# Kernel optimization log

Hardware: AMD Instinct MI355X
Metric: run time of the kernel (lower is better)

Reference implementation:

```python
import jax, jax.numpy as jnp
import numpy as np

INPUT_DIM = 1024
OUTPUT_DIM = 1024
NUM_SEGMENTS = 8
GRID_LO, GRID_HI = -1.0, 1.0


def setup_inputs() -> dict:
    key = jax.random.key(0)
    k1, k2 = jax.random.split(key)
    x = jax.random.normal(k1, (8, 2048, INPUT_DIM), dtype=jnp.float32)
    coeff = jax.random.normal(k2, (NUM_SEGMENTS + 1, OUTPUT_DIM, INPUT_DIM), dtype=jnp.float32) * 0.1
    bias = jnp.zeros((OUTPUT_DIM,), dtype=jnp.float32)
    return {"x": x, "coeff": coeff, "bias": bias}


def reference(x, coeff, bias):
    # x: (..., I); coeff: (G, O, I) with G = num_segments + 1; bias: (O,)
    batch_shape = x.shape[:-1]
    x_flat = x.reshape(-1, INPUT_DIM)                      # (B, I)
    grid = jnp.linspace(GRID_LO, GRID_HI, NUM_SEGMENTS + 1, dtype=x.dtype)  # (G,)
    h = (GRID_HI - GRID_LO) / NUM_SEGMENTS

    x_mean = jnp.mean(x_flat, axis=-1, keepdims=True)      # (B, 1)
    diff = x_mean - grid[None, :]                          # (B, G)
    w = jax.nn.relu(1.0 - jnp.abs(diff) / h)               # triangular hat weights
    w = w / (jnp.sum(w, axis=-1, keepdims=True) + 1e-8)    # (B, G)

    # Fused contraction order: avoid the (B, O, I) intermediate of the
    # original einsum chain; same math by associativity.
    t = jnp.einsum('bi,goi->bgo', x_flat, coeff)           # (B, G, O)
    out = jnp.einsum('bg,bgo->bo', w, t) + bias            # (B, O)
    return out.reshape(*batch_shape, OUTPUT_DIM)
```

## Files before the change

kernel.cpp:

```cpp
#include <hip/hip_runtime.h>
#include <math.h>

#define B_ROWS 16384
#define IDIM   1024
#define ODIM   1024
#define NGRID  9
#define MT_MAX 137
#define MPAD_MAX (MT_MAX*128)

#define RS_BLOCKS 256
#define RS_ROWS   (B_ROWS / RS_BLOCKS)

typedef __attribute__((ext_vector_type(8))) short frag8;
typedef __attribute__((ext_vector_type(4))) float f32x4;

typedef __attribute__((address_space(1))) void gvoid;
typedef __attribute__((address_space(3))) void lvoid;

__device__ __forceinline__ void async_cp16(const void* g, void* l) {
  __builtin_amdgcn_global_load_lds((gvoid*)(void*)g, (lvoid*)l, 16, 0, 0);
}

__device__ __forceinline__ unsigned short f2bf(float f) {
  union { float f; unsigned u; } v; v.f = f;
  unsigned u = v.u;
  u += 0x7fffu + ((u >> 16) & 1u);
  return (unsigned short)(u >> 16);
}

__device__ __forceinline__ void seg_weights(float m, int& sI, float& w0, float& w1) {
  float wsum = 0.f, wg[NGRID];
#pragma unroll
  for (int g = 0; g < NGRID; g++) {
    float gv = -1.f + 0.25f * (float)g;
    float t = 1.f - fabsf(m - gv) * 4.f;
    wg[g] = t > 0.f ? t : 0.f;
    wsum += wg[g];
  }
  int s = (int)floorf((m + 1.f) * 4.f);
  s = s < 0 ? 0 : (s > 7 ? 7 : s);
  float inv = 1.f / (wsum + 1e-8f);
  sI = s;
  w0 = wg[s] * inv;
  w1 = wg[s + 1] * inv;
}

__global__ void zero_meta(int* bucket_cnt) {
  if (threadIdx.x < NGRID) bucket_cnt[threadIdx.x] = 0;
}

__global__ void row_stats(const float* __restrict__ x, float* __restrict__ w0a,
                          float* __restrict__ w1a, int* __restrict__ sidx,
                          int* __restrict__ rank, int* __restrict__ bucket_cnt) {
  __shared__ int lcnt[NGRID];
  __shared__ int base[NGRID];
  __shared__ int lrank[RS_ROWS];
  __shared__ int lseg[RS_ROWS];
  const int tid  = threadIdx.x;
  const int lane = tid & 63;
  const int wave = tid >> 6;
  if (tid < NGRID) lcnt[tid] = 0;
  __syncthreads();
  const int row0 = blockIdx.x * RS_ROWS;
#pragma unroll 4
  for (int it = 0; it < RS_ROWS / 4; ++it) {
    int r = it * 4 + wave;
    int b = row0 + r;
    const float4* xr = (const float4*)(x + (size_t)b * IDIM);
    float s = 0.f;
#pragma unroll
    for (int j = 0; j < 4; j++) {
      float4 v = xr[lane + j * 64];
      s += v.x + v.y + v.z + v.w;
    }
#pragma unroll
    for (int off = 32; off; off >>= 1) s += __shfl_down(s, off, 64);
    if (lane == 0) {
      float m = s * (1.0f / (float)IDIM);
      int sI; float w0, w1;
      seg_weights(m, sI, w0, w1);
      w0a[b] = w0; w1a[b] = w1; sidx[b] = sI;
      lseg[r] = sI;
      lrank[r] = atomicAdd(&lcnt[sI], 1);
    }
  }
  __syncthreads();
  if (tid < NGRID) base[tid] = lcnt[tid] ? atomicAdd(&bucket_cnt[tid], lcnt[tid]) : 0;
  __syncthreads();
  if (tid < RS_ROWS) rank[row0 + tid] = base[lseg[tid]] + lrank[tid];
}

__global__ void plan_kernel(const int* __restrict__ cnt, int* __restrict__ bucket_off,
                            int* __restrict__ tile_seg, int* __restrict__ row_idx) {
  __shared__ int offs[NGRID + 1];
  const int tid = threadIdx.x;
  if (tid == 0) {
    int off = 0;
    for (int g = 0; g < NGRID; g++) {
      offs[g] = off;
      off += ((cnt[g] + 127) >> 7) << 7;
    }
    offs[NGRID] = off;
  }
  __syncthreads();
  if (tid < NGRID) bucket_off[tid] = offs[tid];
  for (int t = tid; t < MT_MAX; t += 256) {
    int seg = -1;
#pragma unroll
    for (int g = 0; g < NGRID; g++)
      if (t >= (offs[g] >> 7) && t < (offs[g + 1] >> 7)) seg = g;
    tile_seg[t] = seg;
  }
#pragma unroll
  for (int g = 0; g < NGRID; g++) {
    int lo = offs[g] + cnt[g], hi = offs[g + 1];
    for (int p = lo + tid; p < hi; p += 256) row_idx[p] = -1;
  }
}

#define BA_ROWS 8
__global__ void build_a(const float* __restrict__ x, const float* __restrict__ w0a,
                        const float* __restrict__ w1a, const int* __restrict__ sidx,
                        const int* __restrict__ rank, const int* __restrict__ bucket_off,
                        unsigned short* __restrict__ Xs, float2* __restrict__ ws,
                        int* __restrict__ row_idx) {
  const int tid = threadIdx.x;
  const int b0 = blockIdx.x * BA_ROWS;
#pragma unroll
  for (int r = 0; r < BA_ROWS; r++) {
    int b = b0 + r;
    int s = sidx[b];
    int p = bucket_off[s] + rank[b];
    if (tid == 0) { row_idx[p] = b; ws[p] = make_float2(w0a[b], w1a[b]); }
    float4 v = ((const float4*)(x + (size_t)b * IDIM))[tid];
    ushort4 u;
    u.x = f2bf(v.x); u.y = f2bf(v.y); u.z = f2bf(v.z); u.w = f2bf(v.w);
    *(ushort4*)(Xs + (size_t)p * IDIM + tid * 4) = u;
  }
}

__global__ void cvt_coeff(const float* __restrict__ c, unsigned short* __restrict__ cb, int n4) {
  int i = blockIdx.x * blockDim.x + threadIdx.x;
  if (i < n4) {
    float4 v = ((const float4*)c)[i];
    ushort4 o;
    o.x = f2bf(v.x); o.y = f2bf(v.y); o.z = f2bf(v.z); o.w = f2bf(v.w);
    ((ushort4*)cb)[i] = o;
  }
}

__global__ void __launch_bounds__(256, 2)
kan_gemm(const unsigned short* __restrict__ Xs,
         const unsigned short* __restrict__ Cb,
         const int* __restrict__ row_idx,
         const int* __restrict__ tile_seg,
         const float2* __restrict__ ws,
         const float* __restrict__ bias,
         float* __restrict__ out) {
  int seg = tile_seg[blockIdx.y];
  if (seg < 0) return;
  __shared__ unsigned short As[128 * 32];
  __shared__ unsigned short Bs0[128 * 32];
  __shared__ unsigned short Bs1[128 * 32];

  const int tid  = threadIdx.x;
  const int lane = tid & 63;
  const int wave = tid >> 6;
  const int wm   = wave >> 1;
  const int wn   = wave & 1;
  const size_t rowA0 = (size_t)blockIdx.y * 128;
  const int    colB0 = blockIdx.x * 128;

  const int lrow = lane >> 2;
  const int lk8  = (lane & 3) * 8;

  const unsigned short* gA  = Xs + (rowA0 + lrow) * IDIM + lk8;
  const unsigned short* gB0 = Cb + ((size_t)(seg * ODIM + colB0 + lrow)) * IDIM + lk8;
  const unsigned short* gB1 = gB0 + (size_t)ODIM * IDIM;

  f32x4 acc0[4][4] = {};
  f32x4 acc1[4][4] = {};

  for (int kk = 0; kk < IDIM; kk += 32) {
    __syncthreads();
#pragma unroll
    for (int t = 0; t < 2; t++) {
      int r0 = (wave * 2 + t) * 16;
      async_cp16(gA  + (size_t)r0 * IDIM + kk, &As[r0 * 32]);
      async_cp16(gB0 + (size_t)r0 * IDIM + kk, &Bs0[r0 * 32]);
      async_cp16(gB1 + (size_t)r0 * IDIM + kk, &Bs1[r0 * 32]);
    }
    __syncthreads();

    frag8 af[4], bfr[4];
#pragma unroll
    for (int mi = 0; mi < 4; mi++)
      af[mi] = *(const frag8*)&As[(wm * 64 + mi * 16 + (lane & 15)) * 32 + (lane >> 4) * 8];
#pragma unroll
    for (int ni = 0; ni < 4; ni++)
      bfr[ni] = *(const frag8*)&Bs0[(wn * 64 + ni * 16 + (lane & 15)) * 32 + (lane >> 4) * 8];
#pragma unroll
    for (int mi = 0; mi < 4; mi++)
#pragma unroll
      for (int ni = 0; ni < 4; ni++)
        acc0[mi][ni] = __builtin_amdgcn_mfma_f32_16x16x32_bf16(af[mi], bfr[ni], acc0[mi][ni], 0, 0, 0);
#pragma unroll
    for (int ni = 0; ni < 4; ni++)
      bfr[ni] = *(const frag8*)&Bs1[(wn * 64 + ni * 16 + (lane & 15)) * 32 + (lane >> 4) * 8];
#pragma unroll
    for (int mi = 0; mi < 4; mi++)
#pragma unroll
      for (int ni = 0; ni < 4; ni++)
        acc1[mi][ni] = __builtin_amdgcn_mfma_f32_16x16x32_bf16(af[mi], bfr[ni], acc1[mi][ni], 0, 0, 0);
  }

  int   col[4]; float bv[4];
#pragma unroll
  for (int ni = 0; ni < 4; ni++) {
    col[ni] = colB0 + wn * 64 + ni * 16 + (lane & 15);
    bv[ni]  = bias[col[ni]];
  }
#pragma unroll
  for (int mi = 0; mi < 4; mi++) {
    int prow = (int)rowA0 + wm * 64 + mi * 16 + (lane >> 4) * 4;
#pragma unroll
    for (int r = 0; r < 4; r++) {
      int p = prow + r;
      int orow = row_idx[p];
      if ((unsigned)orow < (unsigned)B_ROWS) {
        float2 w = ws[p];
        float* o = out + (size_t)orow * ODIM;
#pragma unroll
        for (int ni = 0; ni < 4; ni++)
          o[col[ni]] = w.x * acc0[mi][ni][r] + w.y * acc1[mi][ni][r] + bv[ni];
      }
    }
  }
}

__global__ void fallback_kernel(const float* __restrict__ x, const float* __restrict__ coeff,
                                const float* __restrict__ bias, float* __restrict__ out) {
  int b = blockIdx.x;
  int tid = threadIdx.x;
  __shared__ float xs[IDIM];
  __shared__ float ps[4];
  __shared__ float mw[2];
  __shared__ int   ms;
  float4 v = ((const float4*)(x + (size_t)b * IDIM))[tid];
  ((float4*)xs)[tid] = v;
  float s = v.x + v.y + v.z + v.w;
#pragma unroll
  for (int off = 32; off; off >>= 1) s += __shfl_down(s, off, 64);
  if ((tid & 63) == 0) ps[tid >> 6] = s;
  __syncthreads();
  if (tid == 0) {
    float m = (ps[0] + ps[1] + ps[2] + ps[3]) * (1.0f / (float)IDIM);
    int sI; float w0, w1;
    seg_weights(m, sI, w0, w1);
    mw[0] = w0; mw[1] = w1; ms = sI;
  }
  __syncthreads();
  float w0 = mw[0], w1 = mw[1]; int sI = ms;
  for (int o = tid; o < ODIM; o += 256) {
    const float* c0 = coeff + ((size_t)sI * ODIM + o) * IDIM;
    const float* c1 = c0 + (size_t)ODIM * IDIM;
    float a0 = 0.f, a1 = 0.f;
    for (int i = 0; i < IDIM; i++) { a0 += xs[i] * c0[i]; a1 += xs[i] * c1[i]; }
    out[(size_t)b * ODIM + o] = w0 * a0 + w1 * a1 + bias[o];
  }
}

extern "C" void kernel_launch(void* const* d_in, const int* in_sizes, int n_in,
                              void* d_out, int out_size, void* d_ws, size_t ws_size,
                              hipStream_t stream) {
  const float* x     = (const float*)d_in[0];
  const float* coeff = (const float*)d_in[1];
  const float* bias  = (const float*)d_in[2];
  float* out = (float*)d_out;

  size_t szXs = (size_t)MPAD_MAX * IDIM * sizeof(unsigned short);
  size_t szCb = (size_t)NGRID * ODIM * IDIM * sizeof(unsigned short);
  size_t o0 = 0;
  unsigned short* Xs = (unsigned short*)((char*)d_ws + o0); o0 += szXs;
  unsigned short* Cb = (unsigned short*)((char*)d_ws + o0); o0 += szCb;
  float2* ws = (float2*)((char*)d_ws + o0); o0 += (size_t)MPAD_MAX * 8;
  float* w0a = (float*)((char*)d_ws + o0); o0 += (size_t)B_ROWS * 4;
  float* w1a = (float*)((char*)d_ws + o0); o0 += (size_t)B_ROWS * 4;
  int* sidx  = (int*)((char*)d_ws + o0);   o0 += (size_t)B_ROWS * 4;
  int* rank  = (int*)((char*)d_ws + o0);   o0 += (size_t)B_ROWS * 4;
  int* row_idx = (int*)((char*)d_ws + o0); o0 += (size_t)MPAD_MAX * 4;
  int* bucket_cnt = (int*)((char*)d_ws + o0); o0 += 256;
  int* bucket_off = (int*)((char*)d_ws + o0); o0 += 256;
  int* tile_seg   = (int*)((char*)d_ws + o0); o0 += 1024;

  if (ws_size < o0) {
    fallback_kernel<<<B_ROWS, 256, 0, stream>>>(x, coeff, bias, out);
    return;
  }

  zero_meta<<<1, 64, 0, stream>>>(bucket_cnt);
  row_stats<<<RS_BLOCKS, 256, 0, stream>>>(x, w0a, w1a, sidx, rank, bucket_cnt);
  plan_kernel<<<1, 256, 0, stream>>>(bucket_cnt, bucket_off, tile_seg, row_idx);
  build_a<<<B_ROWS / BA_ROWS, 256, 0, stream>>>(x, w0a, w1a, sidx, rank, bucket_off, Xs, ws, row_idx);
  int n4 = NGRID * ODIM * IDIM / 4;
  cvt_coeff<<<(n4 + 255) / 256, 256, 0, stream>>>(coeff, Cb, n4);
  kan_gemm<<<dim3(ODIM / 128, MT_MAX), 256, 0, stream>>>(Xs, Cb, row_idx, tile_seg, ws, bias, out);
}
```

Before: 278.8 us.

## Fold planning into consumers, merge build and coeff conversion, widen GEMM K-step

Removes the single-block plan kernel. The bucket offsets and tile-to-segment mapping are now recomputed inline, in build_and_cvt and in the GEMM from bucket_cnt. The activation gather/convert and coefficient bf16 conversion become one launch, cutting two kernel launches and their serialization. The GEMM now loads 64 K-elements per barrier pair into doubled shared buffers, halving syncs but raising LDS use, and row_stats uses more blocks with full unroll; padding rows are masked by a computed bound instead of -1 sentinels.

```diff
diff --git a/kernel.cpp b/kernel.cpp
--- a/kernel.cpp
+++ b/kernel.cpp
@@ -8,7 +8,7 @@
 #define MT_MAX 137
 #define MPAD_MAX (MT_MAX*128)
 
-#define RS_BLOCKS 256
+#define RS_BLOCKS 1024
 #define RS_ROWS   (B_ROWS / RS_BLOCKS)
 
 typedef __attribute__((ext_vector_type(8))) short frag8;
@@ -62,7 +62,7 @@
   if (tid < NGRID) lcnt[tid] = 0;
   __syncthreads();
   const int row0 = blockIdx.x * RS_ROWS;
-#pragma unroll 4
+#pragma unroll
   for (int it = 0; it < RS_ROWS / 4; ++it) {
     int r = it * 4 + wave;
     int b = row0 + r;
@@ -90,47 +90,37 @@
   if (tid < RS_ROWS) rank[row0 + tid] = base[lseg[tid]] + lrank[tid];
 }
 
-__global__ void plan_kernel(const int* __restrict__ cnt, int* __restrict__ bucket_off,
-                            int* __restrict__ tile_seg, int* __restrict__ row_idx) {
-  __shared__ int offs[NGRID + 1];
+#define BA_ROWS   8
+#define BA_BLOCKS (B_ROWS / BA_ROWS)
+#define CV_BLOCKS (NGRID * ODIM * IDIM / 4 / 256)
+__global__ void build_and_cvt(const float* __restrict__ x, const float* __restrict__ coeff,
+                              const float* __restrict__ w0a, const float* __restrict__ w1a,
+                              const int* __restrict__ sidx, const int* __restrict__ rank,
+                              const int* __restrict__ bucket_cnt,
+                              unsigned short* __restrict__ Xs, float2* __restrict__ ws,
+                              int* __restrict__ row_idx, unsigned short* __restrict__ Cb) {
   const int tid = threadIdx.x;
+  if (blockIdx.x >= BA_BLOCKS) {
+    int i = (blockIdx.x - BA_BLOCKS) * 256 + tid;
+    float4 v = ((const float4*)coeff)[i];
+    ushort4 o;
+    o.x = f2bf(v.x); o.y = f2bf(v.y); o.z = f2bf(v.z); o.w = f2bf(v.w);
+    ((ushort4*)Cb)[i] = o;
+    return;
+  }
+  __shared__ int soffs[NGRID];
   if (tid == 0) {
     int off = 0;
-    for (int g = 0; g < NGRID; g++) {
-      offs[g] = off;
-      off += ((cnt[g] + 127) >> 7) << 7;
-    }
-    offs[NGRID] = off;
-  }
-  __syncthreads();
-  if (tid < NGRID) bucket_off[tid] = offs[tid];
-  for (int t = tid; t < MT_MAX; t += 256) {
-    int seg = -1;
-#pragma unroll
-    for (int g = 0; g < NGRID; g++)
-      if (t >= (offs[g] >> 7) && t < (offs[g + 1] >> 7)) seg = g;
-    tile_seg[t] = seg;
-  }
-#pragma unroll
-  for (int g = 0; g < NGRID; g++) {
-    int lo = offs[g] + cnt[g], hi = offs[g + 1];
-    for (int p = lo + tid; p < hi; p += 256) row_idx[p] = -1;
-  }
-}
-
-#define BA_ROWS 8
-__global__ void build_a(const float* __restrict__ x, const float* __restrict__ w0a,
-                        const float* __restrict__ w1a, const int* __restrict__ sidx,
-                        const int* __restrict__ rank, const int* __restrict__ bucket_off,
-                        unsigned short* __restrict__ Xs, float2* __restrict__ ws,
-                        int* __restrict__ row_idx) {
-  const int tid = threadIdx.x;
+#pragma unroll
+    for (int g = 0; g < NGRID; g++) { soffs[g] = off; off += ((bucket_cnt[g] + 127) >> 7) << 7; }
+  }
+  __syncthreads();
   const int b0 = blockIdx.x * BA_ROWS;
 #pragma unroll
   for (int r = 0; r < BA_ROWS; r++) {
     int b = b0 + r;
     int s = sidx[b];
-    int p = bucket_off[s] + rank[b];
+    int p = soffs[s] + rank[b];
     if (tid == 0) { row_idx[p] = b; ws[p] = make_float2(w0a[b], w1a[b]); }
     float4 v = ((const float4*)(x + (size_t)b * IDIM))[tid];
     ushort4 u;
@@ -139,36 +129,39 @@
   }
 }
 
-__global__ void cvt_coeff(const float* __restrict__ c, unsigned short* __restrict__ cb, int n4) {
-  int i = blockIdx.x * blockDim.x + threadIdx.x;
-  if (i < n4) {
-    float4 v = ((const float4*)c)[i];
-    ushort4 o;
-    o.x = f2bf(v.x); o.y = f2bf(v.y); o.z = f2bf(v.z); o.w = f2bf(v.w);
-    ((ushort4*)cb)[i] = o;
-  }
-}
-
 __global__ void __launch_bounds__(256, 2)
 kan_gemm(const unsigned short* __restrict__ Xs,
          const unsigned short* __restrict__ Cb,
          const int* __restrict__ row_idx,
-         const int* __restrict__ tile_seg,
+         const int* __restrict__ bucket_cnt,
          const float2* __restrict__ ws,
          const float* __restrict__ bias,
          float* __restrict__ out) {
-  int seg = tile_seg[blockIdx.y];
+  const int mt = blockIdx.y;
+  int seg = -1, pend = 0;
+  {
+    int off = 0;
+#pragma unroll
+    for (int g = 0; g < NGRID; g++) {
+      int c  = bucket_cnt[g];
+      int nt = (c + 127) >> 7;
+      int t0 = off >> 7;
+      if (mt >= t0 && mt < t0 + nt) { seg = g; pend = off + c; }
+      off += nt << 7;
+    }
+  }
   if (seg < 0) return;
-  __shared__ unsigned short As[128 * 32];
-  __shared__ unsigned short Bs0[128 * 32];
-  __shared__ unsigned short Bs1[128 * 32];
+
+  __shared__ unsigned short As[2][128 * 32];
+  __shared__ unsigned short Bs0[2][128 * 32];
+  __shared__ unsigned short Bs1[2][128 * 32];
 
   const int tid  = threadIdx.x;
   const int lane = tid & 63;
   const int wave = tid >> 6;
   const int wm   = wave >> 1;
   const int wn   = wave & 1;
-  const size_t rowA0 = (size_t)blockIdx.y * 128;
+  const size_t rowA0 = (size_t)mt * 128;
   const int    colB0 = blockIdx.x * 128;
 
   const int lrow = lane >> 2;
@@ -181,37 +174,44 @@
   f32x4 acc0[4][4] = {};
   f32x4 acc1[4][4] = {};
 
-  for (int kk = 0; kk < IDIM; kk += 32) {
+  for (int kk = 0; kk < IDIM; kk += 64) {
     __syncthreads();
 #pragma unroll
-    for (int t = 0; t < 2; t++) {
-      int r0 = (wave * 2 + t) * 16;
-      async_cp16(gA  + (size_t)r0 * IDIM + kk, &As[r0 * 32]);
-      async_cp16(gB0 + (size_t)r0 * IDIM + kk, &Bs0[r0 * 32]);
-      async_cp16(gB1 + (size_t)r0 * IDIM + kk, &Bs1[r0 * 32]);
+    for (int h = 0; h < 2; h++) {
+#pragma unroll
+      for (int t = 0; t < 2; t++) {
+        int r0 = (wave * 2 + t) * 16;
+        int ko = kk + h * 32;
+        async_cp16(gA  + (size_t)r0 * IDIM + ko, &As[h][r0 * 32]);
+        async_cp16(gB0 + (size_t)r0 * IDIM + ko, &Bs0[h][r0 * 32]);
+        async_cp16(gB1 + (size_t)r0 * IDIM + ko, &Bs1[h][r0 * 32]);
+      }
     }
     __syncthreads();
 
-    frag8 af[4], bfr[4];
-#pragma unroll
-    for (int mi = 0; mi < 4; mi++)
-      af[mi] = *(const frag8*)&As[(wm * 64 + mi * 16 + (lane & 15)) * 32 + (lane >> 4) * 8];
-#pragma unroll
-    for (int ni = 0; ni < 4; ni++)
-      bfr[ni] = *(const frag8*)&Bs0[(wn * 64 + ni * 16 + (lane & 15)) * 32 + (lane >> 4) * 8];
-#pragma unroll
-    for (int mi = 0; mi < 4; mi++)
+#pragma unroll
+    for (int h = 0; h < 2; h++) {
+      frag8 af[4], bfr[4];
+#pragma unroll
+      for (int mi = 0; mi < 4; mi++)
+        af[mi] = *(const frag8*)&As[h][(wm * 64 + mi * 16 + (lane & 15)) * 32 + (lane >> 4) * 8];
 #pragma unroll
       for (int ni = 0; ni < 4; ni++)
-        acc0[mi][ni] = __builtin_amdgcn_mfma_f32_16x16x32_bf16(af[mi], bfr[ni], acc0[mi][ni], 0, 0, 0);
-#pragma unroll
-    for (int ni = 0; ni < 4; ni++)
-      bfr[ni] = *(const frag8*)&Bs1[(wn * 64 + ni * 16 + (lane & 15)) * 32 + (lane >> 4) * 8];
-#pragma unroll
-    for (int mi = 0; mi < 4; mi++)
+        bfr[ni] = *(const frag8*)&Bs0[h][(wn * 64 + ni * 16 + (lane & 15)) * 32 + (lane >> 4) * 8];
+#pragma unroll
+      for (int mi = 0; mi < 4; mi++)
+#pragma unroll
+        for (int ni = 0; ni < 4; ni++)
+          acc0[mi][ni] = __builtin_amdgcn_mfma_f32_16x16x32_bf16(af[mi], bfr[ni], acc0[mi][ni], 0, 0, 0);
 #pragma unroll
       for (int ni = 0; ni < 4; ni++)
-        acc1[mi][ni] = __builtin_amdgcn_mfma_f32_16x16x32_bf16(af[mi], bfr[ni], acc1[mi][ni], 0, 0, 0);
+        bfr[ni] = *(const frag8*)&Bs1[h][(wn * 64 + ni * 16 + (lane & 15)) * 32 + (lane >> 4) * 8];
+#pragma unroll
+      for (int mi = 0; mi < 4; mi++)
+#pragma unroll
+        for (int ni = 0; ni < 4; ni++)
+          acc1[mi][ni] = __builtin_amdgcn_mfma_f32_16x16x32_bf16(af[mi], bfr[ni], acc1[mi][ni], 0, 0, 0);
+    }
   }
 
   int   col[4]; float bv[4];
@@ -226,8 +226,8 @@
 #pragma unroll
     for (int r = 0; r < 4; r++) {
       int p = prow + r;
-      int orow = row_idx[p];
-      if ((unsigned)orow < (unsigned)B_ROWS) {
+      if (p < pend) {
+        int orow = row_idx[p];
         float2 w = ws[p];
         float* o = out + (size_t)orow * ODIM;
 #pragma unroll
@@ -290,8 +290,6 @@
   int* rank  = (int*)((char*)d_ws + o0);   o0 += (size_t)B_ROWS * 4;
   int* row_idx = (int*)((char*)d_ws + o0); o0 += (size_t)MPAD_MAX * 4;
   int* bucket_cnt = (int*)((char*)d_ws + o0); o0 += 256;
-  int* bucket_off = (int*)((char*)d_ws + o0); o0 += 256;
-  int* tile_seg   = (int*)((char*)d_ws + o0); o0 += 1024;
 
   if (ws_size < o0) {
     fallback_kernel<<<B_ROWS, 256, 0, stream>>>(x, coeff, bias, out);
@@ -300,9 +298,7 @@
 
   zero_meta<<<1, 64, 0, stream>>>(bucket_cnt);
   row_stats<<<RS_BLOCKS, 256, 0, stream>>>(x, w0a, w1a, sidx, rank, bucket_cnt);
-  plan_kernel<<<1, 256, 0, stream>>>(bucket_cnt, bucket_off, tile_seg, row_idx);
-  build_a<<<B_ROWS / BA_ROWS, 256, 0, stream>>>(x, w0a, w1a, sidx, rank, bucket_off, Xs, ws, row_idx);
-  int n4 = NGRID * ODIM * IDIM / 4;
-  cvt_coeff<<<(n4 + 255) / 256, 256, 0, stream>>>(coeff, Cb, n4);
-  kan_gemm<<<dim3(ODIM / 128, MT_MAX), 256, 0, stream>>>(Xs, Cb, row_idx, tile_seg, ws, bias, out);
-}
+  build_and_cvt<<<BA_BLOCKS + CV_BLOCKS, 256, 0, stream>>>(x, coeff, w0a, w1a, sidx, rank,
+                                                           bucket_cnt, Xs, ws, row_idx, Cb);
+  kan_gemm<<<dim3(ODIM / 128, MT_MAX), 256, 0, stream>>>(Xs, Cb, row_idx, bucket_cnt, ws, bias, out);
+}
```

After: 271.5 us. 2.6% less time.
